# Optimization experiments

Hardware: AMD Instinct MI355X
Metric: run time of the kernel (lower is better)

## Reference

```python
import math
import jax, jax.numpy as jnp
import numpy as np

LN_EPS = 1e-5


def _layernorm(x, g, b):
    m = jnp.mean(x, axis=-1, keepdims=True)
    v = jnp.var(x, axis=-1, keepdims=True)
    return (x - m) / jnp.sqrt(v + LN_EPS) * g + b


def setup_inputs() -> dict:
    key = jax.random.key(0)
    ks = jax.random.split(key, 14)
    B, C, H, W = 8, 96, 224, 224
    dim, hidden = 96, int(96 * 4.0)

    def lin(k, i, o):
        return jax.random.normal(k, (i, o), jnp.float32) * 0.02

    return {
        "x": jax.random.normal(ks[0], (B, C, H, W), jnp.float32),
        "entropy_map": jax.random.uniform(ks[1], (B, 1, H, W), jnp.float32),
        "beta": jnp.float32(1.0),
        "wq": lin(ks[2], dim, dim), "bq": jnp.zeros((dim,), jnp.float32),
        "wk": lin(ks[3], dim, dim), "bk": jnp.zeros((dim,), jnp.float32),
        "wv": lin(ks[4], dim, dim), "bv": jnp.zeros((dim,), jnp.float32),
        "wo": lin(ks[5], dim, dim), "bo": jnp.zeros((dim,), jnp.float32),
        "ln1_g": jnp.ones((dim,), jnp.float32), "ln1_b": jnp.zeros((dim,), jnp.float32),
        "ln2_g": jnp.ones((dim,), jnp.float32), "ln2_b": jnp.zeros((dim,), jnp.float32),
        "w_fc1": lin(ks[6], dim, hidden), "b_fc1": jnp.zeros((hidden,), jnp.float32),
        "w_fc2": lin(ks[7], hidden, dim), "b_fc2": jnp.zeros((dim,), jnp.float32),
    }


def reference(x, entropy_map, beta, wq, bq, wk, bk, wv, bv, wo, bo,
              ln1_g, ln1_b, ln2_g, ln2_b, w_fc1, b_fc1, w_fc2, b_fc2):
    B, C, H, W = x.shape
    ws = 7
    num_heads = 4
    hd = C // num_heads
    nHw, nWw = H // ws, W // ws
    N = ws * ws

    # (B,C,H,W) -> (B,H,W,C), norm1
    xt = jnp.transpose(x, (0, 2, 3, 1))
    xn = _layernorm(xt, ln1_g, ln1_b)

    # window partition -> (B*nW, N, C)
    xw = xn.reshape(B, nHw, ws, nWw, ws, C).transpose(0, 1, 3, 2, 4, 5).reshape(-1, N, C)
    ew = entropy_map.transpose(0, 2, 3, 1).reshape(B, nHw, ws, nWw, ws, 1)
    ew = ew.transpose(0, 1, 3, 2, 4, 5).reshape(-1, N, 1)  # (Bw, N, 1)

    Bw = xw.shape[0]
    q = (jnp.einsum('bnc,cd->bnd', xw, wq) + bq).reshape(Bw, N, num_heads, hd).transpose(0, 2, 1, 3)
    k = (jnp.einsum('bnc,cd->bnd', xw, wk) + bk).reshape(Bw, N, num_heads, hd).transpose(0, 2, 1, 3)
    v = (jnp.einsum('bnc,cd->bnd', xw, wv) + bv).reshape(Bw, N, num_heads, hd).transpose(0, 2, 1, 3)

    scores = jnp.einsum('bhqd,bhkd->bhqk', q, k) / math.sqrt(hd)
    attn = jax.nn.softmax(scores, axis=-1)

    # entropy gating: per-query factor (Bw,1,N,1), then renormalize over keys
    gating = jnp.exp(-beta * ew)[:, None, :, :]
    attn = attn * gating
    attn = attn / (jnp.sum(attn, axis=-1, keepdims=True) + 1e-9)

    out = jnp.einsum('bhqk,bhkd->bhqd', attn, v).transpose(0, 2, 1, 3).reshape(Bw, N, C)
    out = jnp.einsum('bnc,cd->bnd', out, wo) + bo

    # window merge -> (B,H,W,C)
    out = out.reshape(B, nHw, nWw, ws, ws, C).transpose(0, 1, 3, 2, 4, 5).reshape(B, H, W, C)

    x_res = xt + out  # (B,H,W,C)

    # MLP branch
    xn2 = _layernorm(x_res, ln2_g, ln2_b)
    h = jax.nn.gelu(jnp.einsum('bhwc,cd->bhwd', xn2, w_fc1) + b_fc1, approximate=False)
    mlp_out = jnp.einsum('bhwd,dc->bhwc', h, w_fc2) + b_fc2

    x_out = x_res + mlp_out
    return jnp.transpose(x_out, (0, 3, 1, 2))  # (B,C,H,W)
```

## Files before the change

kernel.cpp:

```cpp
#include <hip/hip_runtime.h>
#include <math.h>

typedef __attribute__((ext_vector_type(8))) short short8;
typedef __attribute__((ext_vector_type(4))) float f32x4;
typedef __attribute__((ext_vector_type(4))) unsigned int uint4v;

struct __align__(8) U2 { unsigned int x, y; };

#define DEVI static __device__ __forceinline__

DEVI unsigned pk1(float f){ unsigned u = __float_as_uint(f); return (u + 0x7fffu + ((u>>16)&1u)) >> 16; }
DEVI unsigned pk2(float a, float b){ return pk1(a) | (pk1(b) << 16); }
DEVI float bfu(unsigned hs){ return __uint_as_float((hs & 0xffffu) << 16); }

DEVI short8 lds8(const unsigned short* p){
  union { short8 v; U2 u[2]; } f;
  f.u[0] = *(const U2*)p;
  f.u[1] = *(const U2*)(p + 4);
  return f.v;
}
DEVI short8 mk8(unsigned a, unsigned b, unsigned c, unsigned d){
  union { short8 v; unsigned u[4]; } f; f.u[0]=a; f.u[1]=b; f.u[2]=c; f.u[3]=d; return f.v;
}
DEVI short8 zero8(){ return mk8(0,0,0,0); }
DEVI short8 gfrag(const unsigned short* p){ union { short8 v; uint4v u; } f; f.u = *(const uint4v*)p; return f.v; }
DEVI f32x4 MFMA(short8 a, short8 b, f32x4 c){ return __builtin_amdgcn_mfma_f32_16x16x32_bf16(a, b, c, 0, 0, 0); }
DEVI void st2(unsigned short* p, unsigned lo, unsigned hi){ U2 t; t.x=lo; t.y=hi; *(U2*)p = t; }

DEVI float fastrcp(float x){ float r; asm("v_rcp_f32 %0, %1" : "=v"(r) : "v"(x)); return r; }
DEVI float gelu_f(float v){
  float z2 = fmaf(v*v*v, -0.07135481627f, -1.5957691216f*v);
  return v * fastrcp(1.f + __expf(z2));
}

__global__ __launch_bounds__(256) void prep_kernel(
    const float* __restrict__ wq, const float* __restrict__ wk,
    const float* __restrict__ wv, const float* __restrict__ wo,
    const float* __restrict__ w1, const float* __restrict__ w2,
    unsigned short* __restrict__ wfr)
{
  int i = blockIdx.x * 256 + threadIdx.x;
  if (i >= 110592) return;
  int j = i & 7, lane = (i >> 3) & 63, fr = i >> 9;
  int ln = lane & 15, lg = lane >> 4;
  float v;
  if (fr < 18)      { int s = fr;       int mt = s/3,  kb = s%3;  v = wq[(32*kb + 8*lg + j)*96  + 16*mt + ln] * 0.20412414523193150818f; }
  else if (fr < 36) { int s = fr - 18;  int mt = s/3,  kb = s%3;  v = wk[(32*kb + 8*lg + j)*96  + 16*mt + ln]; }
  else if (fr < 54) { int s = fr - 36;  int nt = s/3,  kb = s%3;  v = wv[(32*kb + 8*lg + j)*96  + 16*nt + ln]; }
  else if (fr < 72) { int s = fr - 54;  int mt = s/3,  kb = s%3;  v = wo[(32*kb + 8*lg + j)*96  + 16*mt + ln]; }
  else if (fr < 144){ int s = fr - 72;  int mt = s/3,  kb = s%3;  v = w1[(32*kb + 8*lg + j)*384 + 16*mt + ln]; }
  else              { int s = fr - 144; int mt = s/12, kb = s%12; v = w2[(32*kb + 8*lg + j)*96  + 16*mt + ln]; }
  wfr[i] = (unsigned short)pk1(v);
}

__global__ __launch_bounds__(256, 3) void attn_kernel(
    const float* __restrict__ x, const float* __restrict__ emap,
    const float* __restrict__ beta_p,
    const float* __restrict__ bq, const float* __restrict__ bk,
    const float* __restrict__ bv, const float* __restrict__ bo,
    const float* __restrict__ g1, const float* __restrict__ b1,
    const unsigned short* __restrict__ wfr,
    unsigned short* __restrict__ xres)
{
  __shared__ __align__(16) char smem[52544];
  unsigned short* XN = (unsigned short*)(smem);
  unsigned short* QS = (unsigned short*)(smem + 12800);
  unsigned short* KS = (unsigned short*)(smem + 25600);
  unsigned short* VT = (unsigned short*)(smem + 38400);

  const int tid = threadIdx.x;
  const int lane = tid & 63;
  const int w = tid >> 6, lg = lane >> 4, ln = lane & 15;

  int bid = blockIdx.x;
  int bw  = ((bid & 7) << 10) | (bid >> 3);
  const int b  = bw >> 10;
  const int rr = bw & 1023;
  const int h0 = (rr >> 5) * 7;
  const int w0 = (rr & 31) * 7;

  const int t = 16*w + ln;

  float xv[24];
  float ewv = 0.f;
  {
    if (t < 49){
      size_t pixloc = (size_t)(h0 + t/7)*224 + w0 + t%7;
      const float* xp = x + (size_t)(b*96 + 4*lg)*50176 + pixloc;
#pragma unroll
      for (int mt = 0; mt < 6; ++mt)
#pragma unroll
        for (int r = 0; r < 4; ++r) xv[mt*4+r] = xp[(size_t)(16*mt + r)*50176];
      ewv = emap[(size_t)b*50176 + pixloc];
    } else {
#pragma unroll
      for (int i = 0; i < 24; ++i) xv[i] = 0.f;
    }
    float s = 0.f, s2 = 0.f;
#pragma unroll
    for (int i = 0; i < 24; ++i){ s += xv[i]; s2 += xv[i]*xv[i]; }
    s  += __shfl_xor(s, 16);  s  += __shfl_xor(s, 32);
    s2 += __shfl_xor(s2, 16); s2 += __shfl_xor(s2, 32);
    float m = s * (1.f/96.f);
    float var = s2 * (1.f/96.f) - m*m;
    float rstd = rsqrtf(var + 1e-5f);
    unsigned short* row = XN + t*100;
    if (t < 49){
#pragma unroll
      for (int mt = 0; mt < 6; ++mt){
        int c0 = 16*mt + 4*lg;
        st2(row + c0,
            pk2((xv[4*mt+0]-m)*rstd*g1[c0+0]+b1[c0+0], (xv[4*mt+1]-m)*rstd*g1[c0+1]+b1[c0+1]),
            pk2((xv[4*mt+2]-m)*rstd*g1[c0+2]+b1[c0+2], (xv[4*mt+3]-m)*rstd*g1[c0+3]+b1[c0+3]));
      }
    } else {
#pragma unroll
      for (int mt = 0; mt < 6; ++mt) st2(row + 16*mt + 4*lg, 0u, 0u);
    }
  }
  __syncthreads();

  {
    short8 bx0 = lds8(XN + t*100 + 0  + 8*lg);
    short8 bx1 = lds8(XN + t*100 + 32 + 8*lg);
    short8 bx2 = lds8(XN + t*100 + 64 + 8*lg);
#pragma unroll
    for (int mt = 0; mt < 6; ++mt){
      int d0 = 16*mt + 4*lg;
      f32x4 aq, ak;
#pragma unroll
      for (int r = 0; r < 4; ++r){ aq[r] = bq[d0+r]*0.20412414523193150818f; ak[r] = bk[d0+r]; }
      aq = MFMA(gfrag(wfr +        (mt*3+0)*512 + lane*8), bx0, aq);
      aq = MFMA(gfrag(wfr +        (mt*3+1)*512 + lane*8), bx1, aq);
      aq = MFMA(gfrag(wfr +        (mt*3+2)*512 + lane*8), bx2, aq);
      ak = MFMA(gfrag(wfr + 9216 + (mt*3+0)*512 + lane*8), bx0, ak);
      ak = MFMA(gfrag(wfr + 9216 + (mt*3+1)*512 + lane*8), bx1, ak);
      ak = MFMA(gfrag(wfr + 9216 + (mt*3+2)*512 + lane*8), bx2, ak);
      st2(QS + t*100 + d0, pk2(aq[0],aq[1]), pk2(aq[2],aq[3]));
      st2(KS + t*100 + d0, pk2(ak[0],ak[1]), pk2(ak[2],ak[3]));
    }
#pragma unroll
    for (int f = 0; f < 6; ++f){
      int fl = f*4 + w;
      int mt = fl / 6, nt = fl % 6;
      float bvv = bv[16*nt + ln];
      f32x4 av; av[0]=bvv; av[1]=bvv; av[2]=bvv; av[3]=bvv;
#pragma unroll
      for (int kb = 0; kb < 3; ++kb)
        av = MFMA(lds8(XN + (16*mt+ln)*100 + 32*kb + 8*lg),
                  gfrag(wfr + 18432 + (nt*3+kb)*512 + lane*8), av);
      st2(VT + (16*nt+ln)*68 + 16*mt + 4*lg, pk2(av[0],av[1]), pk2(av[2],av[3]));
    }
  }
  __syncthreads();

  const float beta = beta_p[0];
  const float gq   = __expf(-beta * ewv);
  const float gfac = gq / (gq + 1e-9f);
  const int  psrcA = ((lg & 1) << 5) + ln;
  const int  psrcB = psrcA + 16;
  const bool phi   = (lg >= 2);

  f32x4 mz;  mz[0]=0.f; mz[1]=0.f; mz[2]=0.f; mz[3]=0.f;
  f32x4 m3;
#pragma unroll
  for (int r = 0; r < 4; ++r) m3[r] = (4*lg + r >= 1) ? -50.f : 0.f;

#pragma unroll
  for (int h = 0; h < 4; ++h){
    short8 bqf = (lg < 3) ? lds8(QS + t*100 + 24*h + 8*lg) : zero8();
    f32x4 sva[4];
#pragma unroll
    for (int mt = 0; mt < 4; ++mt){
      short8 af = (lg < 3) ? lds8(KS + (16*mt+ln)*100 + 24*h + 8*lg) : zero8();
      sva[mt] = MFMA(af, bqf, (mt == 3) ? m3 : mz);
    }
    float vv[16]; float ssum = 0.f;
#pragma unroll
    for (int i = 0; i < 16; ++i){ float e = __expf(sva[i>>2][i&3]); vv[i] = e; ssum += e; }
    ssum += __shfl_xor(ssum, 16);
    ssum += __shfl_xor(ssum, 32);
    float inv = gfac * fastrcp(ssum);

    unsigned pu[4][2];
#pragma unroll
    for (int mt = 0; mt < 4; ++mt){
      pu[mt][0] = pk2(vv[4*mt+0], vv[4*mt+1]);
      pu[mt][1] = pk2(vv[4*mt+2], vv[4*mt+3]);
    }
    unsigned a00=__shfl(pu[0][0],psrcA), a01=__shfl(pu[0][1],psrcA);
    unsigned a10=__shfl(pu[1][0],psrcA), a11=__shfl(pu[1][1],psrcA);
    unsigned b00=__shfl(pu[0][0],psrcB), b01=__shfl(pu[0][1],psrcB);
    unsigned b10=__shfl(pu[1][0],psrcB), b11=__shfl(pu[1][1],psrcB);
    short8 pf0 = mk8(phi?a10:a00, phi?a11:a01, phi?b10:b00, phi?b11:b01);
    unsigned c00=__shfl(pu[2][0],psrcA), c01=__shfl(pu[2][1],psrcA);
    unsigned c10=__shfl(pu[3][0],psrcA), c11=__shfl(pu[3][1],psrcA);
    unsigned d00=__shfl(pu[2][0],psrcB), d01=__shfl(pu[2][1],psrcB);
    unsigned d10=__shfl(pu[3][0],psrcB), d11=__shfl(pu[3][1],psrcB);
    short8 pf1 = mk8(phi?c10:c00, phi?c11:c01, phi?d10:d00, phi?d11:d01);

#pragma unroll
    for (int mt = 0; mt < 2; ++mt){
      f32x4 pv; pv[0]=0.f; pv[1]=0.f; pv[2]=0.f; pv[3]=0.f;
      pv = MFMA(lds8(VT + (24*h+16*mt+ln)*68 + 0  + 8*lg), pf0, pv);
      pv = MFMA(lds8(VT + (24*h+16*mt+ln)*68 + 32 + 8*lg), pf1, pv);
      if (!(mt == 1 && lg >= 2))
        st2(XN + t*100 + 24*h + 16*mt + 4*lg,
            pk2(pv[0]*inv, pv[1]*inv), pk2(pv[2]*inv, pv[3]*inv));
    }
  }

  {
    f32x4 po[6];
#pragma unroll
    for (int mt = 0; mt < 6; ++mt){
      int c0 = 16*mt + 4*lg;
#pragma unroll
      for (int r = 0; r < 4; ++r) po[mt][r] = bo[c0+r];
    }
#pragma unroll
    for (int kb = 0; kb < 3; ++kb){
      short8 bf_ = lds8(XN + t*100 + 32*kb + 8*lg);
#pragma unroll
      for (int mt = 0; mt < 6; ++mt)
        po[mt] = MFMA(gfrag(wfr + 27648 + (mt*3+kb)*512 + lane*8), bf_, po[mt]);
    }
    if (t < 49){
      size_t pixloc = (size_t)(h0 + t/7)*224 + w0 + t%7;
      unsigned short* xo = xres + ((size_t)b*50176 + pixloc)*96;
#pragma unroll
      for (int mt = 0; mt < 6; ++mt){
        int c0 = 16*mt + 4*lg;
        st2(xo + c0,
            pk2(po[mt][0] + xv[4*mt+0], po[mt][1] + xv[4*mt+1]),
            pk2(po[mt][2] + xv[4*mt+2], po[mt][3] + xv[4*mt+3]));
      }
    }
  }
}

__global__ __launch_bounds__(256, 4) void mlp_kernel(
    const unsigned short* __restrict__ xres,
    const float* __restrict__ g2, const float* __restrict__ b2,
    const float* __restrict__ bf1, const float* __restrict__ bf2,
    const unsigned short* __restrict__ wfr,
    float* __restrict__ out)
{
  __shared__ __align__(16) unsigned short XH[4][4800];
  const int tid = threadIdx.x, lane = tid & 63, w = tid >> 6;
  const int lg = lane >> 4, ln = lane & 15;
  unsigned short* XN2 = &XH[w][0];
  unsigned short* HS  = &XH[w][1600];

  const int tile = blockIdx.x*4 + w;
  const size_t p0 = (size_t)tile * 16;
  const int bimg = (int)(p0 / 50176);
  const size_t pixin = p0 - (size_t)bimg*50176;

  {
    const unsigned* xp = (const unsigned*)(xres + (p0 + (size_t)ln)*96 + 24*lg);
    float xv[24];
#pragma unroll
    for (int i = 0; i < 12; ++i){
      unsigned u = xp[i];
      xv[2*i] = bfu(u); xv[2*i+1] = bfu(u >> 16);
    }
    float s = 0.f, s2 = 0.f;
#pragma unroll
    for (int i = 0; i < 24; ++i){ s += xv[i]; s2 += xv[i]*xv[i]; }
    s  += __shfl_xor(s, 16);  s  += __shfl_xor(s, 32);
    s2 += __shfl_xor(s2, 16); s2 += __shfl_xor(s2, 32);
    float m = s * (1.f/96.f);
    float var = s2 * (1.f/96.f) - m*m;
    float rstd = rsqrtf(var + 1e-5f);
    unsigned* w32 = (unsigned*)(XN2 + ln*100 + 24*lg);
#pragma unroll
    for (int i = 0; i < 12; ++i){
      int c = 24*lg + 2*i;
      w32[i] = pk2((xv[2*i]   - m)*rstd*g2[c]   + b2[c],
                   (xv[2*i+1] - m)*rstd*g2[c+1] + b2[c+1]);
    }
  }

  f32x4 oacc[6];
#pragma unroll
  for (int mt = 0; mt < 6; ++mt){
    int c0 = 16*mt + 4*lg;
#pragma unroll
    for (int r = 0; r < 4; ++r) oacc[mt][r] = bf2[c0+r];
  }

  short8 bxx0 = lds8(XN2 + ln*100 + 0  + 8*lg);
  short8 bxx1 = lds8(XN2 + ln*100 + 32 + 8*lg);
  short8 bxx2 = lds8(XN2 + ln*100 + 64 + 8*lg);

#pragma unroll
  for (int p = 0; p < 2; ++p){
#pragma unroll
    for (int mt = 0; mt < 12; ++mt){
      int hg = p*192 + 16*mt + 4*lg;
      f32x4 ha;
#pragma unroll
      for (int r = 0; r < 4; ++r) ha[r] = bf1[hg+r];
      ha = MFMA(gfrag(wfr + 36864 + ((p*12+mt)*3+0)*512 + lane*8), bxx0, ha);
      ha = MFMA(gfrag(wfr + 36864 + ((p*12+mt)*3+1)*512 + lane*8), bxx1, ha);
      ha = MFMA(gfrag(wfr + 36864 + ((p*12+mt)*3+2)*512 + lane*8), bxx2, ha);
      st2(HS + ln*200 + 16*mt + 4*lg,
          pk2(gelu_f(ha[0]), gelu_f(ha[1])), pk2(gelu_f(ha[2]), gelu_f(ha[3])));
    }
#pragma unroll
    for (int kb = 0; kb < 6; ++kb){
      short8 bh = lds8(HS + ln*200 + 32*kb + 8*lg);
#pragma unroll
      for (int mt = 0; mt < 6; ++mt)
        oacc[mt] = MFMA(gfrag(wfr + 73728 + (mt*12 + p*6 + kb)*512 + lane*8), bh, oacc[mt]);
    }
  }

  {
    const unsigned short* xr = xres + (p0 + (size_t)ln)*96;
    float* ob = out + (size_t)bimg*96*50176 + pixin + ln;
#pragma unroll
    for (int mt = 0; mt < 6; ++mt){
      int c0 = 16*mt + 4*lg;
      U2 rv = *(const U2*)(xr + c0);
      ob[(size_t)(c0+0)*50176] = oacc[mt][0] + bfu(rv.x);
      ob[(size_t)(c0+1)*50176] = oacc[mt][1] + bfu(rv.x >> 16);
      ob[(size_t)(c0+2)*50176] = oacc[mt][2] + bfu(rv.y);
      ob[(size_t)(c0+3)*50176] = oacc[mt][3] + bfu(rv.y >> 16);
    }
  }
}

extern "C" void kernel_launch(void* const* d_in, const int* in_sizes, int n_in,
                              void* d_out, int out_size, void* d_ws, size_t ws_size,
                              hipStream_t stream) {
  const float* x    = (const float*)d_in[0];
  const float* emap = (const float*)d_in[1];
  const float* beta = (const float*)d_in[2];
  const float* wq   = (const float*)d_in[3];
  const float* bq   = (const float*)d_in[4];
  const float* wk   = (const float*)d_in[5];
  const float* bk   = (const float*)d_in[6];
  const float* wv   = (const float*)d_in[7];
  const float* bv   = (const float*)d_in[8];
  const float* wo   = (const float*)d_in[9];
  const float* bo   = (const float*)d_in[10];
  const float* g1   = (const float*)d_in[11];
  const float* b1   = (const float*)d_in[12];
  const float* g2   = (const float*)d_in[13];
  const float* b2   = (const float*)d_in[14];
  const float* w1   = (const float*)d_in[15];
  const float* bf1  = (const float*)d_in[16];
  const float* w2   = (const float*)d_in[17];
  const float* bf2  = (const float*)d_in[18];

  float* out = (float*)d_out;
  unsigned short* wfr  = (unsigned short*)d_ws;
  unsigned short* xres = (unsigned short*)((char*)d_ws + 262144);

  prep_kernel<<<dim3(432), dim3(256), 0, stream>>>(wq, wk, wv, wo, w1, w2, wfr);
  attn_kernel<<<dim3(8192), dim3(256), 0, stream>>>(
      x, emap, beta, bq, bk, bv, bo, g1, b1, wfr, xres);
  mlp_kernel<<<dim3(6272), dim3(256), 0, stream>>>(
      xres, g2, b2, bf1, bf2, wfr, out);
}
```

Measured before the change: 407.0 us.

## Shrink LDS footprints via aliasing and smaller hidden chunks to raise occupancy

The attention kernel now aliases the V-transpose buffer onto the normalized-input buffer, loading the X fragments into registers before the barrier. It computes V with the same register-resident fragments as Q/K, and writes the attention output into the Q buffer, which cuts shared memory enough to target 4 blocks per CU. The MLP kernel processes the 384-wide hidden layer in four chunks of 96 instead of two of 192, halving its per-wave LDS so it can target 6 blocks. pk2 also switches to the HIP bf16 intrinsic conversion. The tighter launch bounds may force register spills, and the scalar transposed V stores may cause LDS bank conflicts.

```diff
diff --git a/kernel.cpp b/kernel.cpp
--- a/kernel.cpp
+++ b/kernel.cpp
@@ -1,4 +1,5 @@
 #include <hip/hip_runtime.h>
+#include <hip/hip_bf16.h>
 #include <math.h>
 
 typedef __attribute__((ext_vector_type(8))) short short8;
@@ -10,7 +11,10 @@
 #define DEVI static __device__ __forceinline__
 
 DEVI unsigned pk1(float f){ unsigned u = __float_as_uint(f); return (u + 0x7fffu + ((u>>16)&1u)) >> 16; }
-DEVI unsigned pk2(float a, float b){ return pk1(a) | (pk1(b) << 16); }
+DEVI unsigned pk2(float a, float b){
+  __hip_bfloat162 h = __float22bfloat162_rn(float2{a, b});
+  union { __hip_bfloat162 h; unsigned u; } c; c.h = h; return c.u;
+}
 DEVI float bfu(unsigned hs){ return __uint_as_float((hs & 0xffffu) << 16); }
 
 DEVI short8 lds8(const unsigned short* p){
@@ -46,14 +50,14 @@
   float v;
   if (fr < 18)      { int s = fr;       int mt = s/3,  kb = s%3;  v = wq[(32*kb + 8*lg + j)*96  + 16*mt + ln] * 0.20412414523193150818f; }
   else if (fr < 36) { int s = fr - 18;  int mt = s/3,  kb = s%3;  v = wk[(32*kb + 8*lg + j)*96  + 16*mt + ln]; }
-  else if (fr < 54) { int s = fr - 36;  int nt = s/3,  kb = s%3;  v = wv[(32*kb + 8*lg + j)*96  + 16*nt + ln]; }
+  else if (fr < 54) { int s = fr - 36;  int mt = s/3,  kb = s%3;  v = wv[(32*kb + 8*lg + j)*96  + 16*mt + ln]; }
   else if (fr < 72) { int s = fr - 54;  int mt = s/3,  kb = s%3;  v = wo[(32*kb + 8*lg + j)*96  + 16*mt + ln]; }
   else if (fr < 144){ int s = fr - 72;  int mt = s/3,  kb = s%3;  v = w1[(32*kb + 8*lg + j)*384 + 16*mt + ln]; }
   else              { int s = fr - 144; int mt = s/12, kb = s%12; v = w2[(32*kb + 8*lg + j)*96  + 16*mt + ln]; }
   wfr[i] = (unsigned short)pk1(v);
 }
 
-__global__ __launch_bounds__(256, 3) void attn_kernel(
+__global__ __launch_bounds__(256, 4) void attn_kernel(
     const float* __restrict__ x, const float* __restrict__ emap,
     const float* __restrict__ beta_p,
     const float* __restrict__ bq, const float* __restrict__ bk,
@@ -62,11 +66,11 @@
     const unsigned short* __restrict__ wfr,
     unsigned short* __restrict__ xres)
 {
-  __shared__ __align__(16) char smem[52544];
+  __shared__ __align__(16) char smem[39744];
   unsigned short* XN = (unsigned short*)(smem);
-  unsigned short* QS = (unsigned short*)(smem + 12800);
-  unsigned short* KS = (unsigned short*)(smem + 25600);
-  unsigned short* VT = (unsigned short*)(smem + 38400);
+  unsigned short* VT = (unsigned short*)(smem);
+  unsigned short* QS = (unsigned short*)(smem + 14144);
+  unsigned short* KS = (unsigned short*)(smem + 26944);
 
   const int tid = threadIdx.x;
   const int lane = tid & 63;
@@ -118,12 +122,13 @@
       for (int mt = 0; mt < 6; ++mt) st2(row + 16*mt + 4*lg, 0u, 0u);
     }
   }
+
+  short8 bx0 = lds8(XN + t*100 + 0  + 8*lg);
+  short8 bx1 = lds8(XN + t*100 + 32 + 8*lg);
+  short8 bx2 = lds8(XN + t*100 + 64 + 8*lg);
   __syncthreads();
 
   {
-    short8 bx0 = lds8(XN + t*100 + 0  + 8*lg);
-    short8 bx1 = lds8(XN + t*100 + 32 + 8*lg);
-    short8 bx2 = lds8(XN + t*100 + 64 + 8*lg);
 #pragma unroll
     for (int mt = 0; mt < 6; ++mt){
       int d0 = 16*mt + 4*lg;
@@ -140,16 +145,16 @@
       st2(KS + t*100 + d0, pk2(ak[0],ak[1]), pk2(ak[2],ak[3]));
     }
 #pragma unroll
-    for (int f = 0; f < 6; ++f){
-      int fl = f*4 + w;
-      int mt = fl / 6, nt = fl % 6;
-      float bvv = bv[16*nt + ln];
-      f32x4 av; av[0]=bvv; av[1]=bvv; av[2]=bvv; av[3]=bvv;
-#pragma unroll
-      for (int kb = 0; kb < 3; ++kb)
-        av = MFMA(lds8(XN + (16*mt+ln)*100 + 32*kb + 8*lg),
-                  gfrag(wfr + 18432 + (nt*3+kb)*512 + lane*8), av);
-      st2(VT + (16*nt+ln)*68 + 16*mt + 4*lg, pk2(av[0],av[1]), pk2(av[2],av[3]));
+    for (int mt = 0; mt < 6; ++mt){
+      int d0 = 16*mt + 4*lg;
+      f32x4 av;
+#pragma unroll
+      for (int r = 0; r < 4; ++r) av[r] = bv[d0+r];
+      av = MFMA(gfrag(wfr + 18432 + (mt*3+0)*512 + lane*8), bx0, av);
+      av = MFMA(gfrag(wfr + 18432 + (mt*3+1)*512 + lane*8), bx1, av);
+      av = MFMA(gfrag(wfr + 18432 + (mt*3+2)*512 + lane*8), bx2, av);
+#pragma unroll
+      for (int r = 0; r < 4; ++r) VT[(d0+r)*68 + t] = (unsigned short)pk1(av[r]);
     }
   }
   __syncthreads();
@@ -205,7 +210,7 @@
       pv = MFMA(lds8(VT + (24*h+16*mt+ln)*68 + 0  + 8*lg), pf0, pv);
       pv = MFMA(lds8(VT + (24*h+16*mt+ln)*68 + 32 + 8*lg), pf1, pv);
       if (!(mt == 1 && lg >= 2))
-        st2(XN + t*100 + 24*h + 16*mt + 4*lg,
+        st2(QS + t*100 + 24*h + 16*mt + 4*lg,
             pk2(pv[0]*inv, pv[1]*inv), pk2(pv[2]*inv, pv[3]*inv));
     }
   }
@@ -220,7 +225,7 @@
     }
 #pragma unroll
     for (int kb = 0; kb < 3; ++kb){
-      short8 bf_ = lds8(XN + t*100 + 32*kb + 8*lg);
+      short8 bf_ = lds8(QS + t*100 + 32*kb + 8*lg);
 #pragma unroll
       for (int mt = 0; mt < 6; ++mt)
         po[mt] = MFMA(gfrag(wfr + 27648 + (mt*3+kb)*512 + lane*8), bf_, po[mt]);
@@ -239,14 +244,14 @@
   }
 }
 
-__global__ __launch_bounds__(256, 4) void mlp_kernel(
+__global__ __launch_bounds__(256, 6) void mlp_kernel(
     const unsigned short* __restrict__ xres,
     const float* __restrict__ g2, const float* __restrict__ b2,
     const float* __restrict__ bf1, const float* __restrict__ bf2,
     const unsigned short* __restrict__ wfr,
     float* __restrict__ out)
 {
-  __shared__ __align__(16) unsigned short XH[4][4800];
+  __shared__ __align__(16) unsigned short XH[4][3200];
   const int tid = threadIdx.x, lane = tid & 63, w = tid >> 6;
   const int lg = lane >> 4, ln = lane & 15;
   unsigned short* XN2 = &XH[w][0];
@@ -295,25 +300,25 @@
   short8 bxx2 = lds8(XN2 + ln*100 + 64 + 8*lg);
 
 #pragma unroll
-  for (int p = 0; p < 2; ++p){
-#pragma unroll
-    for (int mt = 0; mt < 12; ++mt){
-      int hg = p*192 + 16*mt + 4*lg;
+  for (int p = 0; p < 4; ++p){
+#pragma unroll
+    for (int mt = 0; mt < 6; ++mt){
+      int hg = p*96 + 16*mt + 4*lg;
       f32x4 ha;
 #pragma unroll
       for (int r = 0; r < 4; ++r) ha[r] = bf1[hg+r];
-      ha = MFMA(gfrag(wfr + 36864 + ((p*12+mt)*3+0)*512 + lane*8), bxx0, ha);
-      ha = MFMA(gfrag(wfr + 36864 + ((p*12+mt)*3+1)*512 + lane*8), bxx1, ha);
-      ha = MFMA(gfrag(wfr + 36864 + ((p*12+mt)*3+2)*512 + lane*8), bxx2, ha);
-      st2(HS + ln*200 + 16*mt + 4*lg,
+      ha = MFMA(gfrag(wfr + 36864 + ((p*6+mt)*3+0)*512 + lane*8), bxx0, ha);
+      ha = MFMA(gfrag(wfr + 36864 + ((p*6+mt)*3+1)*512 + lane*8), bxx1, ha);
+      ha = MFMA(gfrag(wfr + 36864 + ((p*6+mt)*3+2)*512 + lane*8), bxx2, ha);
+      st2(HS + ln*100 + 16*mt + 4*lg,
           pk2(gelu_f(ha[0]), gelu_f(ha[1])), pk2(gelu_f(ha[2]), gelu_f(ha[3])));
     }
 #pragma unroll
-    for (int kb = 0; kb < 6; ++kb){
-      short8 bh = lds8(HS + ln*200 + 32*kb + 8*lg);
+    for (int kb = 0; kb < 3; ++kb){
+      short8 bh = lds8(HS + ln*100 + 32*kb + 8*lg);
 #pragma unroll
       for (int mt = 0; mt < 6; ++mt)
-        oacc[mt] = MFMA(gfrag(wfr + 73728 + (mt*12 + p*6 + kb)*512 + lane*8), bh, oacc[mt]);
+        oacc[mt] = MFMA(gfrag(wfr + 73728 + (mt*12 + p*3 + kb)*512 + lane*8), bh, oacc[mt]);
     }
   }
 
```

After: 583.4 us. 43.4% more time.
